# Kernel tuning notes

Hardware: AMD Instinct MI355X
Metric: run time of the kernel (lower is better)

## Reference

```python
import jax, jax.numpy as jnp
import numpy as np

N_ENT = 100000


def setup_inputs() -> dict:
    key = jax.random.key(0)
    ks = jax.random.split(key, 10)
    B, D, O, R, E = 50000, 128, 128, 8, 200000
    return {
        "embeddings": jax.random.normal(ks[0], (N_ENT, D), dtype=jnp.float32),
        "head_e": jax.random.normal(ks[1], (B, D), dtype=jnp.float32),
        "tail_e": jax.random.normal(ks[2], (B, D), dtype=jnp.float32),
        "relation_kernel": jax.random.normal(ks[3], (R, D, O), dtype=jnp.float32),
        "self_kernel": jax.random.normal(ks[4], (D, O), dtype=jnp.float32),
        "edge_val": jax.random.uniform(ks[5], (R, E), dtype=jnp.float32),
        "head_idx": jax.random.randint(ks[6], (B,), 0, N_ENT, dtype=jnp.int32),
        "tail_idx": jax.random.randint(ks[7], (B,), 0, N_ENT, dtype=jnp.int32),
        "edge_src": jax.random.randint(ks[8], (R, E), 0, N_ENT, dtype=jnp.int32),
        "edge_dst": jax.random.randint(ks[9], (R, E), 0, N_ENT, dtype=jnp.int32),
    }


def reference(embeddings, head_e, tail_e, relation_kernel, self_kernel,
              edge_val, head_idx, tail_idx, edge_src, edge_dst):
    # Per-relation SpMM: sum_emb[r, row] = sum_{edges e of r with src=row} val[e] * embeddings[dst[e]]
    def spmm(src, dst, val):
        return jax.ops.segment_sum(embeddings[dst] * val[:, None], src,
                                   num_segments=embeddings.shape[0])
    sum_emb = jax.vmap(spmm)(edge_src, edge_dst, edge_val)  # [R, N, D]

    head_update = jnp.take(sum_emb, head_idx, axis=1)  # [R, B, D]
    tail_update = jnp.take(sum_emb, tail_idx, axis=1)  # [R, B, D]

    head_output = head_e @ self_kernel + jnp.einsum('rbd,rdo->bo', head_update, relation_kernel)
    tail_output = tail_e @ self_kernel + jnp.einsum('rbd,rdo->bo', tail_update, relation_kernel)
    return (jax.nn.sigmoid(head_output), jax.nn.sigmoid(tail_output))
```

## Files before the change

### kernel.cpp

```cpp
#include <hip/hip_runtime.h>
#include <hip/hip_bf16.h>
#include <math.h>

#define N_ENT 100000
#define NB    50000
#define NE    200000
#define RR    8
#define NETOT (RR * NE)
#define NSEG  (RR * N_ENT)

typedef float f32x4  __attribute__((ext_vector_type(4)));
typedef short s16x8  __attribute__((ext_vector_type(8)));

__device__ __forceinline__ void split2(float x, short& h, short& l)
{
    unsigned uh = __float_as_uint(x) & 0xffff0000u;
    h = (short)(uh >> 16);
    float r = x - __uint_as_float(uh);
    l = (short)(__float_as_uint(r) >> 16);
}

__device__ __forceinline__ void glds16(const float* g, float* l)
{
    __builtin_amdgcn_global_load_lds(
        (const __attribute__((address_space(1))) void*)g,
        (__attribute__((address_space(3))) void*)l, 16, 0, 0);
}

__global__ __launch_bounds__(256)
void ktconv_k(const float* __restrict__ rel_k, const float* __restrict__ self_k,
              short* __restrict__ Kth, short* __restrict__ Ktl)
{
    const int r = blockIdx.x;
    const float* src = (r < 8) ? rel_k + (size_t)r * 16384 : self_k;
    short* oh = Kth + (size_t)r * 16384;
    short* ol = Ktl + (size_t)r * 16384;
    for (int i = 0; i < 64; ++i) {
        int ix = i * 256 + threadIdx.x;
        int d = ix >> 7, o = ix & 127;
        short h, l;
        split2(src[ix], h, l);
        oh[o * 128 + d] = h;
        ol[o * 128 + d] = l;
    }
}

template<bool FINAL, bool ACCUM>
__global__ __launch_bounds__(256)
void gemm_mfma_k(const float* __restrict__ X, int xstride,
                 const short* __restrict__ Kth, const short* __restrict__ Ktl,
                 int nkc,
                 const float* __restrict__ Abuf, const int* __restrict__ idx,
                 float* __restrict__ out, int nrows)
{
    __shared__ short Bh[128][136];
    __shared__ short Bl[128][136];

    const int t     = threadIdx.x;
    const int wv    = t >> 6;
    const int lane  = t & 63;
    const int col16 = lane & 15;
    const int g     = lane >> 4;
    const int rowbase = blockIdx.x * 128 + wv * 32;

    f32x4 acc[2][8];
#pragma unroll
    for (int m = 0; m < 2; ++m)
#pragma unroll
        for (int c = 0; c < 8; ++c) acc[m][c] = (f32x4){0.f, 0.f, 0.f, 0.f};

    for (int kc = 0; kc < nkc; ++kc) {
        __syncthreads();
        {
            const s16x8* gh = (const s16x8*)(Kth + (size_t)kc * 16384);
            const s16x8* gl = (const s16x8*)(Ktl + (size_t)kc * 16384);
#pragma unroll
            for (int i = 0; i < 8; ++i) {
                int f = t + i * 256;
                int o = f >> 4, c = f & 15;
                *(s16x8*)&Bh[o][c * 8] = gh[f];
                *(s16x8*)&Bl[o][c * 8] = gl[f];
            }
        }
        __syncthreads();

#pragma unroll
        for (int s = 0; s < 4; ++s) {
            s16x8 ah[2], al[2];
#pragma unroll
            for (int m = 0; m < 2; ++m) {
                int r = rowbase + m * 16 + col16;
                if (r > nrows - 1) r = nrows - 1;
                const float* xp = X + (size_t)r * xstride + kc * 128 + s * 32 + g * 8;
                float4 u0 = *(const float4*)xp;
                float4 u1 = *(const float4*)(xp + 4);
                float u[8] = {u0.x, u0.y, u0.z, u0.w, u1.x, u1.y, u1.z, u1.w};
#pragma unroll
                for (int j = 0; j < 8; ++j) {
                    short h, l; split2(u[j], h, l);
                    ah[m][j] = h; al[m][j] = l;
                }
            }
#pragma unroll
            for (int c = 0; c < 8; ++c) {
                s16x8 bh = *(const s16x8*)&Bh[c * 16 + col16][s * 32 + g * 8];
                s16x8 bl = *(const s16x8*)&Bl[c * 16 + col16][s * 32 + g * 8];
#pragma unroll
                for (int m = 0; m < 2; ++m) {
                    acc[m][c] = __builtin_amdgcn_mfma_f32_16x16x32_bf16(ah[m], bh, acc[m][c], 0, 0, 0);
                    acc[m][c] = __builtin_amdgcn_mfma_f32_16x16x32_bf16(ah[m], bl, acc[m][c], 0, 0, 0);
                    acc[m][c] = __builtin_amdgcn_mfma_f32_16x16x32_bf16(al[m], bh, acc[m][c], 0, 0, 0);
                }
            }
        }
    }

#pragma unroll
    for (int m = 0; m < 2; ++m) {
#pragma unroll
        for (int j = 0; j < 4; ++j) {
            int row = rowbase + m * 16 + g * 4 + j;
            if (row >= nrows) continue;
            float* op = out + (size_t)row * 128;
            if (FINAL) {
                int gi = idx[row];
                const float* Ar = Abuf + (size_t)gi * 128;
#pragma unroll
                for (int c = 0; c < 8; ++c) {
                    int col = c * 16 + col16;
                    float x = acc[m][c][j] + Ar[col];
                    op[col] = 1.f / (1.f + __expf(-x));
                }
            } else if (ACCUM) {
#pragma unroll
                for (int c = 0; c < 8; ++c) {
                    int col = c * 16 + col16;
                    op[col] += acc[m][c][j];
                }
            } else {
#pragma unroll
                for (int c = 0; c < 8; ++c)
                    op[c * 16 + col16] = acc[m][c][j];
            }
        }
    }
}

__global__ __launch_bounds__(256)
void count_k(const int* __restrict__ edge_src, unsigned* __restrict__ cnt,
             unsigned char* __restrict__ rank)
{
    int g = blockIdx.x * 256 + threadIdx.x;
    int r = g / NE;
    int src = edge_src[g];
    unsigned old = atomicAdd(&cnt[r * N_ENT + src], 1u);
    rank[g] = (unsigned char)old;
}

__global__ __launch_bounds__(256)
void scan1_k(const unsigned* __restrict__ cnt, unsigned* __restrict__ offs,
             unsigned* __restrict__ bsum)
{
    __shared__ unsigned s[256];
    const int t = threadIdx.x;
    const int base = blockIdx.x * 1024;
    unsigned v[4], sum = 0;
#pragma unroll
    for (int i = 0; i < 4; ++i) {
        int ix = base + t * 4 + i;
        v[i] = (ix < NSEG) ? cnt[ix] : 0u;
        sum += v[i];
    }
    s[t] = sum; __syncthreads();
    for (int off = 1; off < 256; off <<= 1) {
        unsigned x = (t >= off) ? s[t - off] : 0u;
        __syncthreads();
        s[t] += x;
        __syncthreads();
    }
    unsigned run = s[t] - sum;
#pragma unroll
    for (int i = 0; i < 4; ++i) {
        int ix = base + t * 4 + i;
        if (ix < NSEG) offs[ix] = run;
        run += v[i];
    }
    if (t == 255) bsum[blockIdx.x] = s[255];
}

__global__ __launch_bounds__(256)
void scan2_k(unsigned* __restrict__ bsum, int nb)
{
    __shared__ unsigned s[256];
    __shared__ unsigned carry;
    const int t = threadIdx.x;
    if (t == 0) carry = 0;
    __syncthreads();
    for (int base = 0; base < nb; base += 256) {
        unsigned v = (base + t < nb) ? bsum[base + t] : 0u;
        s[t] = v; __syncthreads();
        for (int off = 1; off < 256; off <<= 1) {
            unsigned x = (t >= off) ? s[t - off] : 0u;
            __syncthreads();
            s[t] += x;
            __syncthreads();
        }
        unsigned tot = s[255];
        unsigned excl = s[t] - v + carry;
        if (base + t < nb) bsum[base + t] = excl;
        __syncthreads();
        if (t == 0) carry += tot;
        __syncthreads();
    }
}

__global__ __launch_bounds__(256)
void scan3_k(unsigned* __restrict__ offs, const unsigned* __restrict__ bsum)
{
    const int base = blockIdx.x * 1024;
    unsigned add = bsum[blockIdx.x];
#pragma unroll
    for (int i = 0; i < 4; ++i) {
        int ix = base + threadIdx.x * 4 + i;
        if (ix < NSEG) offs[ix] += add;
    }
    if (blockIdx.x == 0 && threadIdx.x == 0) offs[NSEG] = NETOT;
}

__global__ __launch_bounds__(256)
void fill_k(const int* __restrict__ edge_src, const int* __restrict__ edge_dst,
            const float* __restrict__ edge_val,
            const unsigned* __restrict__ offs,
            const unsigned char* __restrict__ rank,
            int2* __restrict__ recs)
{
    int g = blockIdx.x * 256 + threadIdx.x;
    int r = g / NE;
    int src = edge_src[g];
    int seg = r * N_ENT + src;
    unsigned pos = offs[seg] + rank[g];
    int2 rec;
    rec.x = edge_dst[g];
    rec.y = __float_as_int(edge_val[g]);
    recs[pos] = rec;
}

template<int NR>
__global__ __launch_bounds__(256)
void segsum_k(const unsigned* __restrict__ offs_r, const int2* __restrict__ recs,
              const float* __restrict__ emb, float* __restrict__ B)
{
    constexpr int T = 4;
    constexpr int SLOTS = NR * T;
    __shared__ float stage[4][SLOTS * 128];

    const int s    = (blockIdx.x * 256 + threadIdx.x) >> 6;
    const int wv   = threadIdx.x >> 6;
    const int lane = threadIdx.x & 63;
    if (s >= N_ENT) return;

    unsigned a[NR]; int n[NR];
#pragma unroll
    for (int j = 0; j < NR; ++j) {
        unsigned lo = offs_r[(size_t)j * N_ENT + s];
        unsigned hi = offs_r[(size_t)j * N_ENT + s + 1];
        a[j] = lo; n[j] = (int)(hi - lo);
    }

    int2 rec[NR][T];
#pragma unroll
    for (int j = 0; j < NR; ++j) {
#pragma unroll
        for (int i = 0; i < T; ++i) {
            int ii = (i < n[j]) ? i : (n[j] - 1);
            if (ii < 0) ii = 0;
            unsigned pos = a[j] + (unsigned)ii;
            if (pos > (unsigned)(NETOT - 1)) pos = NETOT - 1;
            rec[j][i] = recs[pos];
        }
    }

    float* myst = &stage[wv][0];
#pragma unroll
    for (int j = 0; j < NR; ++j) {
#pragma unroll
        for (int ip = 0; ip < T / 2; ++ip) {
            int r0 = rec[j][2 * ip].x;
            int r1 = rec[j][2 * ip + 1].x;
            int row = (lane < 32) ? r0 : r1;
            const float* g = emb + (size_t)row * 128 + (lane & 31) * 4;
            glds16(g, myst + (j * T + 2 * ip) * 128);
        }
    }
    asm volatile("s_waitcnt vmcnt(0)" ::: "memory");
    __builtin_amdgcn_sched_barrier(0);

    float2 acc[NR];
#pragma unroll
    for (int j = 0; j < NR; ++j) acc[j] = (float2){0.f, 0.f};
#pragma unroll
    for (int j = 0; j < NR; ++j)
#pragma unroll
        for (int i = 0; i < T; ++i) {
            float2 y = *(const float2*)&myst[(j * T + i) * 128 + lane * 2];
            float v = (i < n[j]) ? __int_as_float(rec[j][i].y) : 0.f;
            acc[j].x = fmaf(v, y.x, acc[j].x);
            acc[j].y = fmaf(v, y.y, acc[j].y);
        }

#pragma unroll
    for (int j = 0; j < NR; ++j) {
        for (int i = T; i < n[j]; ++i) {
            int2 rc = recs[a[j] + i];
            float v = __int_as_float(rc.y);
            float2 yy = *(const float2*)(emb + (size_t)rc.x * 128 + lane * 2);
            acc[j].x = fmaf(v, yy.x, acc[j].x);
            acc[j].y = fmaf(v, yy.y, acc[j].y);
        }
    }

#pragma unroll
    for (int j = 0; j < NR; ++j)
        *(float2*)(B + ((size_t)s * NR + j) * 128 + lane * 2) = acc[j];
}

static void launch_segsum(int nr, const unsigned* offs_r, const int2* recs,
                          const float* emb, float* B, hipStream_t stream)
{
    dim3 blk(256);
    const int blocks = (N_ENT * 64) / 256;
    switch (nr) {
    case 1: segsum_k<1><<<blocks, blk, 0, stream>>>(offs_r, recs, emb, B); break;
    case 2: segsum_k<2><<<blocks, blk, 0, stream>>>(offs_r, recs, emb, B); break;
    case 3: segsum_k<3><<<blocks, blk, 0, stream>>>(offs_r, recs, emb, B); break;
    default: segsum_k<4><<<blocks, blk, 0, stream>>>(offs_r, recs, emb, B); break;
    }
}

extern "C" void kernel_launch(void* const* d_in, const int* in_sizes, int n_in,
                              void* d_out, int out_size, void* d_ws, size_t ws_size,
                              hipStream_t stream)
{
    const float* emb      = (const float*)d_in[0];
    const float* head_e   = (const float*)d_in[1];
    const float* tail_e   = (const float*)d_in[2];
    const float* rel_k    = (const float*)d_in[3];
    const float* self_k   = (const float*)d_in[4];
    const float* edge_val = (const float*)d_in[5];
    const int*   head_idx = (const int*)d_in[6];
    const int*   tail_idx = (const int*)d_in[7];
    const int*   edge_src = (const int*)d_in[8];
    const int*   edge_dst = (const int*)d_in[9];
    float* out = (float*)d_out;

    char* p = (char*)d_ws;
    auto take = [&](size_t bytes) -> char* {
        char* q = p; p += (bytes + 255) & ~(size_t)255; return q;
    };
    float*         A    = (float*)take((size_t)N_ENT * 128 * sizeof(float));
    int2*          recs = (int2*)take((size_t)NETOT * sizeof(int2));
    unsigned*      cnt  = (unsigned*)take((size_t)NSEG * sizeof(unsigned));
    unsigned*      offs = (unsigned*)take(((size_t)NSEG + 1) * sizeof(unsigned));
    unsigned*      bsum = (unsigned*)take(1024 * sizeof(unsigned));
    unsigned char* rank = (unsigned char*)take((size_t)NETOT);
    short*         Kth  = (short*)take((size_t)9 * 16384 * sizeof(short));
    short*         Ktl  = (short*)take((size_t)9 * 16384 * sizeof(short));
    float*         Bbuf = (float*)p;

    size_t used    = (size_t)(p - (char*)d_ws);
    size_t avail   = (ws_size > used) ? ws_size - used : 0;
    size_t per_rel = (size_t)N_ENT * 128 * sizeof(float);
    int RPG = (int)(avail / per_rel);
    if (RPG > 4) RPG = 4;
    if (RPG < 1) RPG = 1;

    const int NB1 = (NSEG + 1023) / 1024;
    dim3 blk(256);

    ktconv_k<<<9, blk, 0, stream>>>(rel_k, self_k, Kth, Ktl);
    hipMemsetAsync(cnt, 0, (size_t)NSEG * sizeof(unsigned), stream);
    count_k<<<NETOT / 256, blk, 0, stream>>>(edge_src, cnt, rank);
    scan1_k<<<NB1, blk, 0, stream>>>(cnt, offs, bsum);
    scan2_k<<<1, blk, 0, stream>>>(bsum, NB1);
    scan3_k<<<NB1, blk, 0, stream>>>(offs, bsum);
    fill_k<<<NETOT / 256, blk, 0, stream>>>(edge_src, edge_dst, edge_val,
                                            offs, rank, recs);

    const int gy = (N_ENT + 127) / 128;
    int first = 1;
    for (int g0 = 0; g0 < RR; ) {
        int nr = (RR - g0 < RPG) ? RR - g0 : RPG;
        launch_segsum(nr, offs + (size_t)g0 * N_ENT, recs, emb, Bbuf, stream);
        if (first)
            gemm_mfma_k<false, false><<<gy, blk, 0, stream>>>(
                Bbuf, nr * 128,
                Kth + (size_t)g0 * 16384, Ktl + (size_t)g0 * 16384, nr,
                nullptr, nullptr, A, N_ENT);
        else
            gemm_mfma_k<false, true><<<gy, blk, 0, stream>>>(
                Bbuf, nr * 128,
                Kth + (size_t)g0 * 16384, Ktl + (size_t)g0 * 16384, nr,
                nullptr, nullptr, A, N_ENT);
        first = 0;
        g0 += nr;
    }

    const int gb = (NB + 127) / 128;
    gemm_mfma_k<true, false><<<gb, blk, 0, stream>>>(
        head_e, 128, Kth + (size_t)8 * 16384, Ktl + (size_t)8 * 16384, 1,
        A, head_idx, out, NB);
    gemm_mfma_k<true, false><<<gb, blk, 0, stream>>>(
        tail_e, 128, Kth + (size_t)8 * 16384, Ktl + (size_t)8 * 16384, 1,
        A, tail_idx, out + (size_t)NB * 128, NB);
}
```

Before: 616.3 us.

## Fuse per-relation segment sum with relation GEMM into one kernel

Replaces the grouped segsum kernels and their follow-up MFMA GEMMs with a single kernel. Each block gathers the segment sums for 64 entities of one relation into shared memory, then multiplies that tile by the relation kernel using split-bf16 MFMA, and accumulates across all 8 relations in registers. This removes the large intermediate B buffer write and read and several kernel launches. In exchange, the gather now uses plain per-row loads instead of async global-to-LDS staging, the loads get less latency hiding within each row loop, and a block synchronisation is added per relation.

Result: slower. 801.8 us (+30.1%).

```diff
diff --git a/kernel.cpp b/kernel.cpp
--- a/kernel.cpp
+++ b/kernel.cpp
@@ -18,13 +18,6 @@
     h = (short)(uh >> 16);
     float r = x - __uint_as_float(uh);
     l = (short)(__float_as_uint(r) >> 16);
-}
-
-__device__ __forceinline__ void glds16(const float* g, float* l)
-{
-    __builtin_amdgcn_global_load_lds(
-        (const __attribute__((address_space(1))) void*)g,
-        (__attribute__((address_space(3))) void*)l, 16, 0, 0);
 }
 
 __global__ __launch_bounds__(256)
@@ -245,95 +238,114 @@
     recs[pos] = rec;
 }
 
-template<int NR>
-__global__ __launch_bounds__(256)
-void segsum_k(const unsigned* __restrict__ offs_r, const int2* __restrict__ recs,
-              const float* __restrict__ emb, float* __restrict__ B)
-{
-    constexpr int T = 4;
-    constexpr int SLOTS = NR * T;
-    __shared__ float stage[4][SLOTS * 128];
-
-    const int s    = (blockIdx.x * 256 + threadIdx.x) >> 6;
-    const int wv   = threadIdx.x >> 6;
-    const int lane = threadIdx.x & 63;
-    if (s >= N_ENT) return;
-
-    unsigned a[NR]; int n[NR];
-#pragma unroll
-    for (int j = 0; j < NR; ++j) {
-        unsigned lo = offs_r[(size_t)j * N_ENT + s];
-        unsigned hi = offs_r[(size_t)j * N_ENT + s + 1];
-        a[j] = lo; n[j] = (int)(hi - lo);
-    }
-
-    int2 rec[NR][T];
-#pragma unroll
-    for (int j = 0; j < NR; ++j) {
-#pragma unroll
-        for (int i = 0; i < T; ++i) {
-            int ii = (i < n[j]) ? i : (n[j] - 1);
-            if (ii < 0) ii = 0;
-            unsigned pos = a[j] + (unsigned)ii;
-            if (pos > (unsigned)(NETOT - 1)) pos = NETOT - 1;
-            rec[j][i] = recs[pos];
-        }
-    }
-
-    float* myst = &stage[wv][0];
-#pragma unroll
-    for (int j = 0; j < NR; ++j) {
-#pragma unroll
-        for (int ip = 0; ip < T / 2; ++ip) {
-            int r0 = rec[j][2 * ip].x;
-            int r1 = rec[j][2 * ip + 1].x;
-            int row = (lane < 32) ? r0 : r1;
-            const float* g = emb + (size_t)row * 128 + (lane & 31) * 4;
-            glds16(g, myst + (j * T + 2 * ip) * 128);
-        }
-    }
-    asm volatile("s_waitcnt vmcnt(0)" ::: "memory");
-    __builtin_amdgcn_sched_barrier(0);
-
-    float2 acc[NR];
-#pragma unroll
-    for (int j = 0; j < NR; ++j) acc[j] = (float2){0.f, 0.f};
-#pragma unroll
-    for (int j = 0; j < NR; ++j)
-#pragma unroll
-        for (int i = 0; i < T; ++i) {
-            float2 y = *(const float2*)&myst[(j * T + i) * 128 + lane * 2];
-            float v = (i < n[j]) ? __int_as_float(rec[j][i].y) : 0.f;
-            acc[j].x = fmaf(v, y.x, acc[j].x);
-            acc[j].y = fmaf(v, y.y, acc[j].y);
-        }
-
-#pragma unroll
-    for (int j = 0; j < NR; ++j) {
-        for (int i = T; i < n[j]; ++i) {
-            int2 rc = recs[a[j] + i];
-            float v = __int_as_float(rc.y);
-            float2 yy = *(const float2*)(emb + (size_t)rc.x * 128 + lane * 2);
-            acc[j].x = fmaf(v, yy.x, acc[j].x);
-            acc[j].y = fmaf(v, yy.y, acc[j].y);
-        }
-    }
-
-#pragma unroll
-    for (int j = 0; j < NR; ++j)
-        *(float2*)(B + ((size_t)s * NR + j) * 128 + lane * 2) = acc[j];
-}
-
-static void launch_segsum(int nr, const unsigned* offs_r, const int2* recs,
-                          const float* emb, float* B, hipStream_t stream)
-{
-    dim3 blk(256);
-    const int blocks = (N_ENT * 64) / 256;
-    switch (nr) {
-    case 1: segsum_k<1><<<blocks, blk, 0, stream>>>(offs_r, recs, emb, B); break;
-    case 2: segsum_k<2><<<blocks, blk, 0, stream>>>(offs_r, recs, emb, B); break;
-    case 3: segsum_k<3><<<blocks, blk, 0, stream>>>(offs_r, recs, emb, B); break;
-    default: segsum_k<4><<<blocks, blk, 0, stream>>>(offs_r, recs, emb, B); break;
+__global__ __launch_bounds__(256)
+void fuse_k(const unsigned* __restrict__ offs, const int2* __restrict__ recs,
+            const float* __restrict__ emb,
+            const short* __restrict__ Kth, const short* __restrict__ Ktl,
+            float* __restrict__ A)
+{
+    __shared__ float X[64][132];
+
+    const int t     = threadIdx.x;
+    const int wv    = t >> 6;
+    const int lane  = t & 63;
+    const int col16 = lane & 15;
+    const int g     = lane >> 4;
+    const int s0    = blockIdx.x * 64;
+    const int mrow  = (wv >> 1) * 32;
+    const int ccol  = (wv & 1) * 64;
+
+    f32x4 acc[2][4];
+#pragma unroll
+    for (int m = 0; m < 2; ++m)
+#pragma unroll
+        for (int c = 0; c < 4; ++c) acc[m][c] = (f32x4){0.f, 0.f, 0.f, 0.f};
+
+    for (int j = 0; j < RR; ++j) {
+        const int segbase = j * N_ENT + s0 + wv * 16;
+#pragma unroll 2
+        for (int row = 0; row < 16; ++row) {
+            int seg = segbase + row;
+            float a0 = 0.f, a1 = 0.f;
+            if (seg < NSEG) {
+                unsigned a = offs[seg];
+                unsigned b = offs[seg + 1];
+                int n = (int)(b - a);
+                int2 rc[4];
+#pragma unroll
+                for (int i = 0; i < 4; ++i) {
+                    int ii = (i < n) ? i : (n - 1);
+                    if (ii < 0) ii = 0;
+                    unsigned pos = a + (unsigned)ii;
+                    if (pos > (unsigned)(NETOT - 1)) pos = NETOT - 1;
+                    rc[i] = recs[pos];
+                }
+#pragma unroll
+                for (int i = 0; i < 4; ++i) {
+                    float2 y = *(const float2*)(emb + (size_t)rc[i].x * 128 + lane * 2);
+                    float v = (i < n) ? __int_as_float(rc[i].y) : 0.f;
+                    a0 = fmaf(v, y.x, a0);
+                    a1 = fmaf(v, y.y, a1);
+                }
+                for (int i = 4; i < n; ++i) {
+                    int2 rc2 = recs[a + (unsigned)i];
+                    float v = __int_as_float(rc2.y);
+                    float2 y = *(const float2*)(emb + (size_t)rc2.x * 128 + lane * 2);
+                    a0 = fmaf(v, y.x, a0);
+                    a1 = fmaf(v, y.y, a1);
+                }
+            }
+            *(float2*)&X[wv * 16 + row][lane * 2] = (float2){a0, a1};
+        }
+
+        __syncthreads();
+
+        const short* KH = Kth + (size_t)j * 16384;
+        const short* KL = Ktl + (size_t)j * 16384;
+#pragma unroll
+        for (int s = 0; s < 4; ++s) {
+            s16x8 bh[4], bl[4];
+#pragma unroll
+            for (int c = 0; c < 4; ++c) {
+                int oo = ccol + c * 16 + col16;
+                int k = s * 32 + g * 8;
+                bh[c] = *(const s16x8*)(KH + (size_t)oo * 128 + k);
+                bl[c] = *(const s16x8*)(KL + (size_t)oo * 128 + k);
+            }
+#pragma unroll
+            for (int m = 0; m < 2; ++m) {
+                const float* xp = &X[mrow + m * 16 + col16][s * 32 + g * 8];
+                float4 u0 = *(const float4*)xp;
+                float4 u1 = *(const float4*)(xp + 4);
+                float u[8] = {u0.x, u0.y, u0.z, u0.w, u1.x, u1.y, u1.z, u1.w};
+                s16x8 ah, al;
+#pragma unroll
+                for (int q = 0; q < 8; ++q) {
+                    short h, l; split2(u[q], h, l);
+                    ah[q] = h; al[q] = l;
+                }
+#pragma unroll
+                for (int c = 0; c < 4; ++c) {
+                    acc[m][c] = __builtin_amdgcn_mfma_f32_16x16x32_bf16(ah, bh[c], acc[m][c], 0, 0, 0);
+                    acc[m][c] = __builtin_amdgcn_mfma_f32_16x16x32_bf16(ah, bl[c], acc[m][c], 0, 0, 0);
+                    acc[m][c] = __builtin_amdgcn_mfma_f32_16x16x32_bf16(al, bh[c], acc[m][c], 0, 0, 0);
+                }
+            }
+        }
+        __syncthreads();
+    }
+
+#pragma unroll
+    for (int m = 0; m < 2; ++m) {
+#pragma unroll
+        for (int jj = 0; jj < 4; ++jj) {
+            int row = s0 + mrow + m * 16 + g * 4 + jj;
+            if (row >= N_ENT) continue;
+            float* op = A + (size_t)row * 128 + ccol;
+#pragma unroll
+            for (int c = 0; c < 4; ++c)
+                op[c * 16 + col16] = acc[m][c][jj];
+        }
     }
 }
 
@@ -365,14 +377,6 @@
     unsigned char* rank = (unsigned char*)take((size_t)NETOT);
     short*         Kth  = (short*)take((size_t)9 * 16384 * sizeof(short));
     short*         Ktl  = (short*)take((size_t)9 * 16384 * sizeof(short));
-    float*         Bbuf = (float*)p;
-
-    size_t used    = (size_t)(p - (char*)d_ws);
-    size_t avail   = (ws_size > used) ? ws_size - used : 0;
-    size_t per_rel = (size_t)N_ENT * 128 * sizeof(float);
-    int RPG = (int)(avail / per_rel);
-    if (RPG > 4) RPG = 4;
-    if (RPG < 1) RPG = 1;
 
     const int NB1 = (NSEG + 1023) / 1024;
     dim3 blk(256);
@@ -386,24 +390,8 @@
     fill_k<<<NETOT / 256, blk, 0, stream>>>(edge_src, edge_dst, edge_val,
                                             offs, rank, recs);
 
-    const int gy = (N_ENT + 127) / 128;
-    int first = 1;
-    for (int g0 = 0; g0 < RR; ) {
-        int nr = (RR - g0 < RPG) ? RR - g0 : RPG;
-        launch_segsum(nr, offs + (size_t)g0 * N_ENT, recs, emb, Bbuf, stream);
-        if (first)
-            gemm_mfma_k<false, false><<<gy, blk, 0, stream>>>(
-                Bbuf, nr * 128,
-                Kth + (size_t)g0 * 16384, Ktl + (size_t)g0 * 16384, nr,
-                nullptr, nullptr, A, N_ENT);
-        else
-            gemm_mfma_k<false, true><<<gy, blk, 0, stream>>>(
-                Bbuf, nr * 128,
-                Kth + (size_t)g0 * 16384, Ktl + (size_t)g0 * 16384, nr,
-                nullptr, nullptr, A, N_ENT);
-        first = 0;
-        g0 += nr;
-    }
+    const int gf = (N_ENT + 63) / 64;
+    fuse_k<<<gf, blk, 0, stream>>>(offs, recs, emb, Kth, Ktl, A);
 
     const int gb = (NB + 127) / 128;
     gemm_mfma_k<true, false><<<gb, blk, 0, stream>>>(
```
